# Performance work log

Measured on AMD Instinct MI355X. Metric: run time of the kernel, lower is better.

The kernel has to match this reference:

```python
import jax, jax.numpy as jnp
import numpy as np

B, C, H, W = 16, 684, 32, 128
HID, A, COV = 256, 512, 512  # hidden_size, attention_dim, attention_conv out-channels


def setup_inputs() -> dict:
    key = jax.random.key(0)
    ks = jax.random.split(key, 12)
    inp = {
        "cnn_features": jax.random.normal(ks[0], (B, C, H, W), jnp.float32),
        "cnn_features_trans": jax.random.normal(ks[1], (B, A, H, W), jnp.float32),
        "hidden": jax.random.normal(ks[2], (B, HID), jnp.float32),
        "alpha_sum": jax.random.uniform(ks[3], (B, 1, H, W), jnp.float32),
        "image_mask": jnp.ones((B, 1, H, W), jnp.int32),
        "counting_map_trans": jax.random.normal(ks[4], (B, H, W, A), jnp.float32),
        # learned params (torch Linear weight is [out,in]; Conv2d weight is [O,I,kh,kw])
        "W_hidden": jax.random.normal(ks[5], (A, HID), jnp.float32) * 0.02,
        "b_hidden": jnp.zeros((A,), jnp.float32),
        "W_attconv": jax.random.normal(ks[6], (COV, 1, 11, 11), jnp.float32) * 0.02,
        "W_attn": jax.random.normal(ks[7], (A, COV), jnp.float32) * 0.02,
        "W_alpha": jax.random.normal(ks[8], (1, A), jnp.float32) * 0.02,
        "b_alpha": jnp.zeros((1,), jnp.float32),
    }
    return inp


def reference(cnn_features, cnn_features_trans, hidden, alpha_sum, image_mask,
              counting_map_trans, W_hidden, b_hidden, W_attconv, W_attn, W_alpha, b_alpha):
    b, c, h, w = cnn_features.shape
    # query = hidden_weight(hidden)  -> [b, A]
    query = hidden @ W_hidden.T + b_hidden
    # alpha_sum_trans = attention_conv(alpha_sum): 11x11 conv, pad 5, no bias -> [b, COV, h, w]
    ast = jax.lax.conv_general_dilated(
        alpha_sum, W_attconv, window_strides=(1, 1), padding=[(5, 5), (5, 5)],
        dimension_numbers=("NCHW", "OIHW", "NCHW"))
    # coverage_alpha = attention_weight(ast.permute(0,2,3,1)) -> [b, h, w, A]
    coverage = jnp.einsum("bkhw,ak->bhwa", ast, W_attn)
    # broadcast add + tanh: [b,h,w,A]
    score = jnp.tanh(query[:, None, None, :] + coverage
                     + cnn_features_trans.transpose(0, 2, 3, 1) + counting_map_trans)
    # energy = alpha_convert(score) -> [b,h,w]
    energy = jnp.einsum("bhwa,a->bhw", score, W_alpha[0]) + b_alpha[0]
    energy = energy - energy.max()  # global max, as in the torch code
    mask = image_mask[:, 0].astype(bool)  # [b,h,w]
    energy = jnp.where(mask, energy, -jnp.inf)
    alpha = jax.nn.softmax(energy.reshape(b, h * w), axis=-1).reshape(b, 1, h, w)
    alpha_sum_new = alpha + alpha_sum
    # context_vector = sum over spatial of alpha * cnn_features -> [b, c]
    context_vector = jnp.einsum("bhw,bchw->bc", alpha[:, 0], cnn_features)
    return context_vector, alpha[:, 0], alpha_sum_new
```

## Files before the change

### kernel.cpp

```cpp
#include <hip/hip_runtime.h>
#include <math.h>

namespace {
constexpr int NB   = 16;
constexpr int NC   = 684;
constexpr int NH   = 32;
constexpr int NW   = 128;
constexpr int NHID = 256;
constexpr int NA   = 512;
constexpr int HW   = NH * NW;
}

__device__ __forceinline__ float fast_tanh(float x) {
  float e = __expf(2.0f * x);
  return 1.0f - 2.0f / (e + 1.0f);
}

__global__ __launch_bounds__(512) void query_kernel(
    const float* __restrict__ hidden, const float* __restrict__ Wh,
    const float* __restrict__ bh, float* __restrict__ q) {
  const int b = blockIdx.x, a = threadIdx.x;
  const float4* h4 = reinterpret_cast<const float4*>(hidden + b * NHID);
  const float4* w4 = reinterpret_cast<const float4*>(Wh + (size_t)a * NHID);
  float s = bh[a];
  #pragma unroll 8
  for (int k = 0; k < NHID / 4; ++k) {
    float4 hv = h4[k], wv = w4[k];
    s = fmaf(hv.x, wv.x, s); s = fmaf(hv.y, wv.y, s);
    s = fmaf(hv.z, wv.z, s); s = fmaf(hv.w, wv.w, s);
  }
  q[b * NA + a] = s;
}

__global__ __launch_bounds__(192) void m_kernel(
    const float* __restrict__ Wattn, const float* __restrict__ Wc,
    float* __restrict__ M) {
  const int a = blockIdx.x, t = threadIdx.x;
  if (t >= 132) return;
  const int dy = t / 12, dx = t % 12;
  float s = 0.0f;
  if (dx < 11) {
    const int j = dy * 11 + dx;
    const float* wa = Wattn + (size_t)a * 512;
    for (int k = 0; k < 512; ++k) s = fmaf(wa[k], Wc[k * 121 + j], s);
  }
  M[(size_t)a * 132 + t] = s;
}

__global__ __launch_bounds__(256) void energy_kernel(
    const float* __restrict__ cft,
    const float* __restrict__ cmt,
    const float* __restrict__ asum,
    const float* __restrict__ q,
    const float* __restrict__ M,
    const float* __restrict__ walpha,
    float* __restrict__ energy)
{
  const int blk  = blockIdx.x;
  const int b    = blk >> 5;
  const int h    = blk & 31;
  const int tid  = threadIdx.x;
  const int lane = tid & 63;
  const int wave = __builtin_amdgcn_readfirstlane(tid >> 6);

  __shared__ float asum_lds[11][144];
  __shared__ float cmt_lds[4][16][NW];
  __shared__ float part[4][NW];

  for (int i = tid; i < 11 * 144; i += 256) {
    const int r = i / 144, cc = i % 144;
    const int y = h + r - 5, x = cc - 5;
    float v = 0.0f;
    if (y >= 0 && y < NH && x >= 0 && x < NW) v = asum[(b * NH + y) * NW + x];
    asum_lds[r][cc] = v;
  }
  __syncthreads();

  const int w0 = lane, w1 = lane + 64;
  float acc0 = 0.0f, acc1 = 0.0f;
  const int abase = wave * 128;
  const float* cmt_base = cmt + (size_t)(b * NH + h) * NW * NA;
  const float* q_b = q + b * NA;
  const int wl = lane >> 2;
  const int a4 = (lane & 3) << 2;

  for (int ab = 0; ab < 8; ++ab) {
    const int a16 = abase + ab * 16;

    #pragma unroll
    for (int p = 0; p < 8; ++p) {
      const int w = p * 16 + wl;
      const float4 v = *reinterpret_cast<const float4*>(
          cmt_base + (size_t)w * NA + (a16 + a4));
      cmt_lds[wave][a4 + 0][w] = v.x;
      cmt_lds[wave][a4 + 1][w] = v.y;
      cmt_lds[wave][a4 + 2][w] = v.z;
      cmt_lds[wave][a4 + 3][w] = v.w;
    }

    float cov0[16], cov1[16];
    #pragma unroll
    for (int i = 0; i < 16; ++i) { cov0[i] = 0.0f; cov1[i] = 0.0f; }

    for (int dy = 0; dy < 11; ++dy) {
      float p0[11], p1[11];
      #pragma unroll
      for (int dx = 0; dx < 11; ++dx) {
        p0[dx] = asum_lds[dy][w0 + dx];
        p1[dx] = asum_lds[dy][w1 + dx];
      }
      #pragma unroll
      for (int ai = 0; ai < 16; ++ai) {
        const float4* mr = reinterpret_cast<const float4*>(
            M + (size_t)(a16 + ai) * 132 + dy * 12);
        const float4 m0 = mr[0];
        const float4 m1 = mr[1];
        const float4 m2 = mr[2];
        float c0 = cov0[ai], c1 = cov1[ai];
        c0 = fmaf(p0[0], m0.x, c0);  c1 = fmaf(p1[0], m0.x, c1);
        c0 = fmaf(p0[1], m0.y, c0);  c1 = fmaf(p1[1], m0.y, c1);
        c0 = fmaf(p0[2], m0.z, c0);  c1 = fmaf(p1[2], m0.z, c1);
        c0 = fmaf(p0[3], m0.w, c0);  c1 = fmaf(p1[3], m0.w, c1);
        c0 = fmaf(p0[4], m1.x, c0);  c1 = fmaf(p1[4], m1.x, c1);
        c0 = fmaf(p0[5], m1.y, c0);  c1 = fmaf(p1[5], m1.y, c1);
        c0 = fmaf(p0[6], m1.z, c0);  c1 = fmaf(p1[6], m1.z, c1);
        c0 = fmaf(p0[7], m1.w, c0);  c1 = fmaf(p1[7], m1.w, c1);
        c0 = fmaf(p0[8], m2.x, c0);  c1 = fmaf(p1[8], m2.x, c1);
        c0 = fmaf(p0[9], m2.y, c0);  c1 = fmaf(p1[9], m2.y, c1);
        c0 = fmaf(p0[10], m2.z, c0); c1 = fmaf(p1[10], m2.z, c1);
        cov0[ai] = c0; cov1[ai] = c1;
      }
    }

    #pragma unroll
    for (int ai = 0; ai < 16; ++ai) {
      const int a = a16 + ai;
      const float qa = q_b[a];
      const float wa = walpha[a];
      const float* cr = cft + ((size_t)(b * NA + a) * NH + h) * NW;
      const float e0 = qa + cov0[ai] + cr[w0] + cmt_lds[wave][ai][w0];
      const float e1 = qa + cov1[ai] + cr[w1] + cmt_lds[wave][ai][w1];
      acc0 = fmaf(wa, fast_tanh(e0), acc0);
      acc1 = fmaf(wa, fast_tanh(e1), acc1);
    }
  }

  part[wave][w0] = acc0;
  part[wave][w1] = acc1;
  __syncthreads();
  if (tid < NW) {
    energy[(b * NH + h) * NW + tid] =
        part[0][tid] + part[1][tid] + part[2][tid] + part[3][tid];
  }
}

__global__ __launch_bounds__(256) void softmax_kernel(
    float* __restrict__ energy_alpha,
    const int* __restrict__ mask,
    const float* __restrict__ asum,
    float* __restrict__ asum_new)
{
  const int b = blockIdx.x, tid = threadIdx.x;
  const int base = b * HW;
  __shared__ float redm[4];
  __shared__ float reds[4];

  float mx = -1e30f;
  for (int i = tid; i < HW; i += 256) {
    float e = energy_alpha[base + i];
    e = mask[base + i] ? e : -1e30f;
    mx = fmaxf(mx, e);
  }
  #pragma unroll
  for (int o = 32; o > 0; o >>= 1) mx = fmaxf(mx, __shfl_down(mx, o));
  if ((tid & 63) == 0) redm[tid >> 6] = mx;
  __syncthreads();
  mx = fmaxf(fmaxf(redm[0], redm[1]), fmaxf(redm[2], redm[3]));

  float s = 0.0f;
  for (int i = tid; i < HW; i += 256) {
    const float e = energy_alpha[base + i];
    s += mask[base + i] ? expf(e - mx) : 0.0f;
  }
  #pragma unroll
  for (int o = 32; o > 0; o >>= 1) s += __shfl_down(s, o);
  if ((tid & 63) == 0) reds[tid >> 6] = s;
  __syncthreads();
  s = reds[0] + reds[1] + reds[2] + reds[3];
  const float inv = 1.0f / s;

  for (int i = tid; i < HW; i += 256) {
    const float e = energy_alpha[base + i];
    const float a = mask[base + i] ? expf(e - mx) * inv : 0.0f;
    energy_alpha[base + i] = a;
    asum_new[base + i] = a + asum[base + i];
  }
}

__global__ __launch_bounds__(256) void context_kernel(
    const float* __restrict__ cnn, const float* __restrict__ alpha,
    float* __restrict__ out) {
  const int blk = blockIdx.x;
  const int b = blk / NC, c = blk - b * NC;
  const float4* crow = reinterpret_cast<const float4*>(cnn + (size_t)(b * NC + c) * HW);
  const float4* arow = reinterpret_cast<const float4*>(alpha + (size_t)b * HW);
  const int tid = threadIdx.x;
  float s = 0.0f;
  #pragma unroll
  for (int i = tid; i < HW / 4; i += 256) {
    const float4 cv = crow[i];
    const float4 av = arow[i];
    s = fmaf(cv.x, av.x, s); s = fmaf(cv.y, av.y, s);
    s = fmaf(cv.z, av.z, s); s = fmaf(cv.w, av.w, s);
  }
  #pragma unroll
  for (int o = 32; o > 0; o >>= 1) s += __shfl_down(s, o);
  __shared__ float red[4];
  if ((tid & 63) == 0) red[tid >> 6] = s;
  __syncthreads();
  if (tid == 0) out[blk] = red[0] + red[1] + red[2] + red[3];
}

extern "C" void kernel_launch(void* const* d_in, const int* in_sizes, int n_in,
                              void* d_out, int out_size, void* d_ws, size_t ws_size,
                              hipStream_t stream) {
  const float* cnn    = (const float*)d_in[0];
  const float* cft    = (const float*)d_in[1];
  const float* hidden = (const float*)d_in[2];
  const float* asum   = (const float*)d_in[3];
  const int*   mask   = (const int*)  d_in[4];
  const float* cmt    = (const float*)d_in[5];
  const float* Wh     = (const float*)d_in[6];
  const float* bh     = (const float*)d_in[7];
  const float* Wc     = (const float*)d_in[8];
  const float* Wattn  = (const float*)d_in[9];
  const float* Walpha = (const float*)d_in[10];

  float* out_ctx   = (float*)d_out;
  float* out_alpha = out_ctx + NB * NC;
  float* out_asum  = out_alpha + NB * HW;

  float* ws_q = (float*)d_ws;
  float* ws_M = ws_q + NB * NA;

  query_kernel<<<NB, 512, 0, stream>>>(hidden, Wh, bh, ws_q);
  m_kernel<<<NA, 192, 0, stream>>>(Wattn, Wc, ws_M);
  energy_kernel<<<NB * NH, 256, 0, stream>>>(cft, cmt, asum, ws_q, ws_M, Walpha, out_alpha);
  softmax_kernel<<<NB, 256, 0, stream>>>(out_alpha, mask, asum, out_asum);
  context_kernel<<<NB * NC, 256, 0, stream>>>(cnn, out_alpha, out_ctx);
}
```

Before: 619.6 us.

## Split energy kernel over attention-dim halves and drop LDS transpose of counting map

The energy kernel now launches twice as many blocks, each handling half of the 512 attention channels and writing a partial energy sum to its own buffer. The softmax kernel adds the two partials, keeps values and mask in registers, and reuses the exponentials instead of re-reading and recomputing them. Counting-map values are loaded directly per thread as float4 instead of being transposed through LDS, and the feature loads are hoisted ahead of the convolution loop. This raises occupancy across CUs and removes LDS traffic, at the cost of an extra workspace buffer and strided per-thread global loads of the counting map.

```diff
diff --git a/kernel.cpp b/kernel.cpp
--- a/kernel.cpp
+++ b/kernel.cpp
@@ -54,17 +54,19 @@
     const float* __restrict__ q,
     const float* __restrict__ M,
     const float* __restrict__ walpha,
-    float* __restrict__ energy)
+    float* __restrict__ epart0,
+    float* __restrict__ epart1)
 {
   const int blk  = blockIdx.x;
-  const int b    = blk >> 5;
-  const int h    = blk & 31;
+  const int half = blk & 1;
+  const int bh   = blk >> 1;
+  const int b    = bh >> 5;
+  const int h    = bh & 31;
   const int tid  = threadIdx.x;
   const int lane = tid & 63;
   const int wave = __builtin_amdgcn_readfirstlane(tid >> 6);
 
   __shared__ float asum_lds[11][144];
-  __shared__ float cmt_lds[4][16][NW];
   __shared__ float part[4][NW];
 
   for (int i = tid; i < 11 * 144; i += 256) {
@@ -77,31 +79,33 @@
   __syncthreads();
 
   const int w0 = lane, w1 = lane + 64;
+  const int abase = half * 256 + wave * 64;
+  const float* q_b = q + b * NA;
+  const float* cmt_row0 = cmt + (size_t)((b * NH + h) * NW + w0) * NA;
+  const float* cmt_row1 = cmt + (size_t)((b * NH + h) * NW + w1) * NA;
+
   float acc0 = 0.0f, acc1 = 0.0f;
-  const int abase = wave * 128;
-  const float* cmt_base = cmt + (size_t)(b * NH + h) * NW * NA;
-  const float* q_b = q + b * NA;
-  const int wl = lane >> 2;
-  const int a4 = (lane & 3) << 2;
 
   for (int ab = 0; ab < 8; ++ab) {
-    const int a16 = abase + ab * 16;
-
-    #pragma unroll
-    for (int p = 0; p < 8; ++p) {
-      const int w = p * 16 + wl;
-      const float4 v = *reinterpret_cast<const float4*>(
-          cmt_base + (size_t)w * NA + (a16 + a4));
-      cmt_lds[wave][a4 + 0][w] = v.x;
-      cmt_lds[wave][a4 + 1][w] = v.y;
-      cmt_lds[wave][a4 + 2][w] = v.z;
-      cmt_lds[wave][a4 + 3][w] = v.w;
+    const int a8 = abase + ab * 8;
+
+    const float4 cma0 = *reinterpret_cast<const float4*>(cmt_row0 + a8);
+    const float4 cma1 = *reinterpret_cast<const float4*>(cmt_row0 + a8 + 4);
+    const float4 cmb0 = *reinterpret_cast<const float4*>(cmt_row1 + a8);
+    const float4 cmb1 = *reinterpret_cast<const float4*>(cmt_row1 + a8 + 4);
+    float cf0[8], cf1[8];
+    #pragma unroll
+    for (int ai = 0; ai < 8; ++ai) {
+      const float* cr = cft + ((size_t)(b * NA + a8 + ai) * NH + h) * NW;
+      cf0[ai] = cr[w0];
+      cf1[ai] = cr[w1];
     }
 
-    float cov0[16], cov1[16];
-    #pragma unroll
-    for (int i = 0; i < 16; ++i) { cov0[i] = 0.0f; cov1[i] = 0.0f; }
-
+    float cov0[8], cov1[8];
+    #pragma unroll
+    for (int i = 0; i < 8; ++i) { cov0[i] = 0.0f; cov1[i] = 0.0f; }
+
+    #pragma unroll
     for (int dy = 0; dy < 11; ++dy) {
       float p0[11], p1[11];
       #pragma unroll
@@ -110,9 +114,9 @@
         p1[dx] = asum_lds[dy][w1 + dx];
       }
       #pragma unroll
-      for (int ai = 0; ai < 16; ++ai) {
+      for (int ai = 0; ai < 8; ++ai) {
         const float4* mr = reinterpret_cast<const float4*>(
-            M + (size_t)(a16 + ai) * 132 + dy * 12);
+            M + (size_t)(a8 + ai) * 132 + dy * 12);
         const float4 m0 = mr[0];
         const float4 m1 = mr[1];
         const float4 m2 = mr[2];
@@ -132,14 +136,17 @@
       }
     }
 
-    #pragma unroll
-    for (int ai = 0; ai < 16; ++ai) {
-      const int a = a16 + ai;
+    const float cm0[8] = {cma0.x, cma0.y, cma0.z, cma0.w,
+                          cma1.x, cma1.y, cma1.z, cma1.w};
+    const float cm1[8] = {cmb0.x, cmb0.y, cmb0.z, cmb0.w,
+                          cmb1.x, cmb1.y, cmb1.z, cmb1.w};
+    #pragma unroll
+    for (int ai = 0; ai < 8; ++ai) {
+      const int a = a8 + ai;
       const float qa = q_b[a];
       const float wa = walpha[a];
-      const float* cr = cft + ((size_t)(b * NA + a) * NH + h) * NW;
-      const float e0 = qa + cov0[ai] + cr[w0] + cmt_lds[wave][ai][w0];
-      const float e1 = qa + cov1[ai] + cr[w1] + cmt_lds[wave][ai][w1];
+      const float e0 = qa + cov0[ai] + cf0[ai] + cm0[ai];
+      const float e1 = qa + cov1[ai] + cf1[ai] + cm1[ai];
       acc0 = fmaf(wa, fast_tanh(e0), acc0);
       acc1 = fmaf(wa, fast_tanh(e1), acc1);
     }
@@ -148,14 +155,16 @@
   part[wave][w0] = acc0;
   part[wave][w1] = acc1;
   __syncthreads();
+  float* epart = half ? epart1 : epart0;
   if (tid < NW) {
-    energy[(b * NH + h) * NW + tid] =
+    epart[(b * NH + h) * NW + tid] =
         part[0][tid] + part[1][tid] + part[2][tid] + part[3][tid];
   }
 }
 
 __global__ __launch_bounds__(256) void softmax_kernel(
-    float* __restrict__ energy_alpha,
+    float* __restrict__ epart0_alpha,
+    const float* __restrict__ epart1,
     const int* __restrict__ mask,
     const float* __restrict__ asum,
     float* __restrict__ asum_new)
@@ -165,11 +174,15 @@
   __shared__ float redm[4];
   __shared__ float reds[4];
 
+  float ev[16];
+  bool mv[16];
   float mx = -1e30f;
-  for (int i = tid; i < HW; i += 256) {
-    float e = energy_alpha[base + i];
-    e = mask[base + i] ? e : -1e30f;
-    mx = fmaxf(mx, e);
+  #pragma unroll
+  for (int k = 0; k < 16; ++k) {
+    const int i = base + tid + k * 256;
+    ev[k] = epart0_alpha[i] + epart1[i];
+    mv[k] = mask[i] != 0;
+    mx = fmaxf(mx, mv[k] ? ev[k] : -1e30f);
   }
   #pragma unroll
   for (int o = 32; o > 0; o >>= 1) mx = fmaxf(mx, __shfl_down(mx, o));
@@ -178,9 +191,11 @@
   mx = fmaxf(fmaxf(redm[0], redm[1]), fmaxf(redm[2], redm[3]));
 
   float s = 0.0f;
-  for (int i = tid; i < HW; i += 256) {
-    const float e = energy_alpha[base + i];
-    s += mask[base + i] ? expf(e - mx) : 0.0f;
+  float pv[16];
+  #pragma unroll
+  for (int k = 0; k < 16; ++k) {
+    pv[k] = mv[k] ? expf(ev[k] - mx) : 0.0f;
+    s += pv[k];
   }
   #pragma unroll
   for (int o = 32; o > 0; o >>= 1) s += __shfl_down(s, o);
@@ -189,11 +204,12 @@
   s = reds[0] + reds[1] + reds[2] + reds[3];
   const float inv = 1.0f / s;
 
-  for (int i = tid; i < HW; i += 256) {
-    const float e = energy_alpha[base + i];
-    const float a = mask[base + i] ? expf(e - mx) * inv : 0.0f;
-    energy_alpha[base + i] = a;
-    asum_new[base + i] = a + asum[base + i];
+  #pragma unroll
+  for (int k = 0; k < 16; ++k) {
+    const int i = base + tid + k * 256;
+    const float a = pv[k] * inv;
+    epart0_alpha[i] = a;
+    asum_new[i] = a + asum[i];
   }
 }
 
@@ -240,12 +256,14 @@
   float* out_alpha = out_ctx + NB * NC;
   float* out_asum  = out_alpha + NB * HW;
 
-  float* ws_q = (float*)d_ws;
-  float* ws_M = ws_q + NB * NA;
+  float* ws_q  = (float*)d_ws;
+  float* ws_M  = ws_q + NB * NA;
+  float* ws_e1 = ws_M + NA * 132;
 
   query_kernel<<<NB, 512, 0, stream>>>(hidden, Wh, bh, ws_q);
   m_kernel<<<NA, 192, 0, stream>>>(Wattn, Wc, ws_M);
-  energy_kernel<<<NB * NH, 256, 0, stream>>>(cft, cmt, asum, ws_q, ws_M, Walpha, out_alpha);
-  softmax_kernel<<<NB, 256, 0, stream>>>(out_alpha, mask, asum, out_asum);
+  energy_kernel<<<NB * NH * 2, 256, 0, stream>>>(cft, cmt, asum, ws_q, ws_M, Walpha,
+                                                 out_alpha, ws_e1);
+  softmax_kernel<<<NB, 256, 0, stream>>>(out_alpha, ws_e1, mask, asum, out_asum);
   context_kernel<<<NB * NC, 256, 0, stream>>>(cnn, out_alpha, out_ctx);
 }
```

New measurement: 1.094 ms. 1.77x slower.
